# Performance work log

Hardware: AMD Instinct MI355X
Metric: run time of the kernel (lower is better)

The kernel has to match this reference:

```python
import jax, jax.numpy as jnp
import numpy as np

NUM_HEADS = 16
NUM_HIDDENS = 1024
NEG_INF = -1e6


def setup_inputs() -> dict:
    key = jax.random.key(0)
    ks = jax.random.split(key, 8)
    B, S, D = 2, 2048, NUM_HIDDENS
    scale = 1.0 / np.sqrt(D)
    return {
        "q": jax.random.normal(ks[0], (B, S, D), jnp.float32),
        "k": jax.random.normal(ks[1], (B, S, D), jnp.float32),
        "v": jax.random.normal(ks[2], (B, S, D), jnp.float32),
        # nn.Linear weights have shape (out_features, in_features)
        "Wq": jax.random.normal(ks[3], (D, D), jnp.float32) * scale,
        "Wk": jax.random.normal(ks[4], (D, D), jnp.float32) * scale,
        "Wv": jax.random.normal(ks[5], (D, D), jnp.float32) * scale,
        "Wo": jax.random.normal(ks[6], (D, D), jnp.float32) * scale,
        "valid_len": jax.random.randint(ks[7], (B,), 1, 2048 + 1, jnp.int32),
    }


def _unpack_heads(x, nh):
    # (B, S, H) -> (B*nh, S, H//nh), matching Unpack_base_head
    B, S, H = x.shape
    return x.reshape(B, S, nh, H // nh).transpose(0, 2, 1, 3).reshape(B * nh, S, H // nh)


def _merge_heads(x, nh):
    # Faithful to Merge_base_head: (B*nh, S, dh) -> (B, nh, S, dh)
    # -> permute(0,2,3,1) -> (B, S, dh, nh) -> (B, S, dh*nh)
    Bnh, S, dh = x.shape
    B = Bnh // nh
    x = x.reshape(B, nh, S, dh).transpose(0, 2, 3, 1)
    return x.reshape(B, S, dh * nh)


def reference(q, k, v, Wq, Wk, Wv, Wo, valid_len):
    nh = NUM_HEADS
    # projections (bias=False); Linear: x @ W.T
    qh = _unpack_heads(q @ Wq.T, nh)  # (B*nh, S, dh)
    kh = _unpack_heads(k @ Wk.T, nh)
    vh = _unpack_heads(v @ Wv.T, nh)
    dh = qh.shape[-1]
    scores = jnp.einsum("bqd,bkd->bqk", qh, kh) / jnp.sqrt(jnp.float32(dh))
    # repeat_interleave valid_len by num_heads along dim 0
    vl = jnp.repeat(valid_len, nh)  # (B*nh,)
    key_pos = jnp.arange(scores.shape[-1])  # (S,)
    mask = key_pos[None, None, :] < vl[:, None, None]  # (B*nh, 1, S)
    scores = jnp.where(mask, scores, NEG_INF)
    attn = jax.nn.softmax(scores, axis=-1)  # dropout=0.0 (eval) -> identity
    out = jnp.einsum("bqk,bkd->bqd", attn, vh)  # (B*nh, S, dh)
    out = _merge_heads(out, nh) @ Wo.T  # (B, S, H)
    return out, attn
```

## Files before the change

### kernel.cpp

```cpp
#include <hip/hip_runtime.h>
#include <stdint.h>

#define SB 2048
#define DB 1024
#define NHB 16
#define DHB 64

typedef __attribute__((ext_vector_type(8))) short short8;
typedef __attribute__((ext_vector_type(4))) short short4v;
typedef __attribute__((ext_vector_type(4))) float f32x4;

#define SC2 0.18033688011112042f

__device__ __forceinline__ unsigned short f2bf(float f) {
  union { float f; uint32_t u; } v; v.f = f;
  uint32_t u = v.u;
  return (unsigned short)((u + 0x7FFFu + ((u >> 16) & 1u)) >> 16);
}

__device__ __forceinline__ void gld16(const void* g, void* l) {
  __builtin_amdgcn_global_load_lds(
      (const __attribute__((address_space(1))) void*)g,
      (__attribute__((address_space(3))) void*)l, 16, 0, 0);
}

__device__ __forceinline__ int xcd_swz(int bid, int nwg) {
  return (bid & 7) * (nwg >> 3) + (bid >> 3);
}

struct ConvArgs {
  const float* s[7];
  unsigned short* d[7];
  int n[7];
};

__global__ __launch_bounds__(256) void conv_kernel(ConvArgs a) {
  const int t = blockIdx.y;
  const float* __restrict__ src = a.s[t];
  unsigned short* __restrict__ dst = a.d[t];
  const int n8 = a.n[t] >> 3;
  for (int i = blockIdx.x * 256 + threadIdx.x; i < n8; i += gridDim.x * 256) {
    const f32x4* p = (const f32x4*)src + (size_t)i * 2;
    f32x4 x = p[0], y = p[1];
    short8 o;
    o[0] = (short)f2bf(x[0]); o[1] = (short)f2bf(x[1]);
    o[2] = (short)f2bf(x[2]); o[3] = (short)f2bf(x[3]);
    o[4] = (short)f2bf(y[0]); o[5] = (short)f2bf(y[1]);
    o[6] = (short)f2bf(y[2]); o[7] = (short)f2bf(y[3]);
    *(short8*)(dst + (size_t)i * 8) = o;
  }
}

struct GemmArgs {
  const unsigned short* A[3];
  const unsigned short* B[3];
  void* O[3];
  int mode[3];
};

__global__ __launch_bounds__(256) void gemm128(GemmArgs ga) {
  __shared__ unsigned short SH[17408];
  unsigned short* Ab = SH;
  unsigned short* Bb = SH + 8192;

  const int z = blockIdx.y;
  const unsigned short* __restrict__ A = ga.A[z];
  const unsigned short* __restrict__ Bw = ga.B[z];
  const int mode = ga.mode[z];

  const int tid = threadIdx.x;
  const int w = tid >> 6, lane = tid & 63;
  const int g = lane >> 4, li = lane & 15;
  const int wm = w >> 1, wn = w & 1;
  const int l = xcd_swz(blockIdx.x, 256);
  const int m0 = (l >> 3) * 128, n0 = (l & 7) * 128;

  const int srow = lane >> 3;
  const int sg = (lane & 7) ^ srow;

  f32x4 acc[4][4];
  #pragma unroll
  for (int i = 0; i < 4; ++i)
    #pragma unroll
    for (int j = 0; j < 4; ++j)
      #pragma unroll
      for (int e = 0; e < 4; ++e) acc[i][j][e] = 0.f;

  for (int k0 = 0; k0 < DB; k0 += 64) {
    __syncthreads();
    #pragma unroll
    for (int i = 0; i < 4; ++i) {
      int c = w * 4 + i;
      gld16(A + (size_t)(m0 + c * 8 + srow) * DB + k0 + sg * 8, Ab + c * 512);
      gld16(Bw + (size_t)(n0 + c * 8 + srow) * DB + k0 + sg * 8, Bb + c * 512);
    }
    __syncthreads();
    short8 af[4][2], bf[4][2];
    #pragma unroll
    for (int mf = 0; mf < 4; ++mf)
      #pragma unroll
      for (int ks = 0; ks < 2; ++ks)
        af[mf][ks] = *(const short8*)&Ab[(wm * 64 + mf * 16 + li) * 64 +
                                         (((ks * 4 + g) ^ (li & 7)) << 3)];
    #pragma unroll
    for (int nf = 0; nf < 4; ++nf)
      #pragma unroll
      for (int ks = 0; ks < 2; ++ks)
        bf[nf][ks] = *(const short8*)&Bb[(wn * 64 + nf * 16 + li) * 64 +
                                         (((ks * 4 + g) ^ (li & 7)) << 3)];
    __builtin_amdgcn_s_setprio(1);
    #pragma unroll
    for (int ks = 0; ks < 2; ++ks)
      #pragma unroll
      for (int mf = 0; mf < 4; ++mf)
        #pragma unroll
        for (int nf = 0; nf < 4; ++nf)
          acc[mf][nf] = __builtin_amdgcn_mfma_f32_16x16x32_bf16(
              af[mf][ks], bf[nf][ks], acc[mf][nf], 0, 0, 0);
    __builtin_amdgcn_s_setprio(0);
  }

  if (mode == 0) {
    unsigned short* O = (unsigned short*)ga.O[z];
    #pragma unroll
    for (int mf = 0; mf < 4; ++mf)
      #pragma unroll
      for (int nf = 0; nf < 4; ++nf)
        #pragma unroll
        for (int r = 0; r < 4; ++r) {
          int row = m0 + wm * 64 + mf * 16 + g * 4 + r;
          int col = n0 + wn * 64 + nf * 16 + li;
          int b_ = row >> 11, s_ = row & 2047;
          int h = col >> 6, dp = col & 63;
          O[((size_t)(b_ * NHB + h) * SB + s_) * DHB + dp] = f2bf(acc[mf][nf][r]);
        }
  } else {
    unsigned short* O = (unsigned short*)ga.O[z];
    __syncthreads();
    #pragma unroll
    for (int mf = 0; mf < 4; ++mf)
      #pragma unroll
      for (int nf = 0; nf < 4; ++nf) {
        short4v pk;
        #pragma unroll
        for (int r = 0; r < 4; ++r) pk[r] = (short)f2bf(acc[mf][nf][r]);
        *(short4v*)&SH[(size_t)(wn * 64 + nf * 16 + li) * 136 +
                       wm * 64 + mf * 16 + g * 4] = pk;
      }
    __syncthreads();
    int c = tid >> 1, rh = tid & 1;
    int col = n0 + c;
    int h = col >> 6, dp = col & 63;
    int b_ = m0 >> 11, s0 = (m0 & 2047) + rh * 64;
    unsigned short* dst = O + ((size_t)(b_ * NHB + h) * DHB + dp) * SB + s0;
    #pragma unroll
    for (int j = 0; j < 8; ++j)
      *(short8*)(dst + j * 8) = *(const short8*)&SH[c * 136 + rh * 64 + j * 8];
  }
}

__global__ __launch_bounds__(256) void attn_kernel(
    const unsigned short* __restrict__ Qh, const unsigned short* __restrict__ Kh,
    const unsigned short* __restrict__ Vt, const int* __restrict__ valid_len,
    float* __restrict__ attn_out, unsigned short* __restrict__ Mg)
{
  __shared__ unsigned short Kb[4096];
  __shared__ unsigned short Vb[4096];
  __shared__ unsigned short QP[64][88];

  const int tid = threadIdx.x;
  const int wave = tid >> 6, lane = tid & 63;
  const int g = lane >> 4, li = lane & 15;
  const int lsw = xcd_swz(blockIdx.x, 1024);
  const int xcd = lsw >> 7, j = lsw & 127;
  const int bh = ((j >> 6) << 4) + xcd * 2 + ((j >> 5) & 1);
  const int q0 = (j & 31) * 64;
  const int b_ = bh >> 4;
  const int vl = valid_len[b_];
  const int nkt = min(32, (vl + 63) >> 6);

  const int srow = lane >> 3;
  const int sg = (lane & 7) ^ srow;

  {
    int qr = tid >> 2, cs = (tid & 3) * 16;
    const unsigned short* src = Qh + ((size_t)bh * SB + q0 + qr) * DHB + cs;
    *(short8*)&QP[qr][cs]     = *(const short8*)src;
    *(short8*)&QP[qr][cs + 8] = *(const short8*)(src + 8);
  }
  __syncthreads();

  short8 qa[2];
  #pragma unroll
  for (int ks = 0; ks < 2; ++ks)
    qa[ks] = *(const short8*)&QP[wave * 16 + li][ks * 32 + g * 8];

  float lQ = 0.f;

  for (int kti = 0; kti < nkt; ++kti) {
    const int kt = kti * 64;
    __syncthreads();
    {
      int c = wave * 2;
      gld16(Kh + ((size_t)bh * SB + kt + c * 8 + srow) * DHB + sg * 8,
            &Kb[c * 512]);
      gld16(Kh + ((size_t)bh * SB + kt + (c + 1) * 8 + srow) * DHB + sg * 8,
            &Kb[(c + 1) * 512]);
    }
    __syncthreads();
    f32x4 sc[4];
    #pragma unroll
    for (int nf = 0; nf < 4; ++nf)
      #pragma unroll
      for (int e = 0; e < 4; ++e) sc[nf][e] = 0.f;
    __builtin_amdgcn_s_setprio(1);
    #pragma unroll
    for (int ks = 0; ks < 2; ++ks)
      #pragma unroll
      for (int nf = 0; nf < 4; ++nf) {
        short8 kbf = *(const short8*)&Kb[(nf * 16 + li) * 64 +
                                         (((ks * 4 + g) ^ (li & 7)) << 3)];
        sc[nf] = __builtin_amdgcn_mfma_f32_16x16x32_bf16(kbf, qa[ks], sc[nf], 0, 0, 0);
      }
    __builtin_amdgcn_s_setprio(0);
    float la = 0.f;
    #pragma unroll
    for (int nf = 0; nf < 4; ++nf)
      #pragma unroll
      for (int r = 0; r < 4; ++r) {
        int key = kt + nf * 16 + g * 4 + r;
        float s2 = (key < vl) ? sc[nf][r] * SC2 : -1.5e6f;
        la += exp2f(s2);
      }
    lQ += la;
  }

  float L = lQ;
  L += __shfl_xor(L, 16);
  L += __shfl_xor(L, 32);
  const float rlQ = 1.f / L;

  f32x4 oacc[4];
  #pragma unroll
  for (int nf = 0; nf < 4; ++nf)
    #pragma unroll
    for (int e = 0; e < 4; ++e) oacc[nf][e] = 0.f;

  for (int kti = 0; kti < nkt; ++kti) {
    const int kt = kti * 64;
    __syncthreads();
    {
      int c = wave * 2;
      gld16(Kh + ((size_t)bh * SB + kt + c * 8 + srow) * DHB + sg * 8,
            &Kb[c * 512]);
      gld16(Kh + ((size_t)bh * SB + kt + (c + 1) * 8 + srow) * DHB + sg * 8,
            &Kb[(c + 1) * 512]);
      gld16(Vt + ((size_t)bh * DHB + c * 8 + srow) * SB + kt + sg * 8,
            &Vb[c * 512]);
      gld16(Vt + ((size_t)bh * DHB + (c + 1) * 8 + srow) * SB + kt + sg * 8,
            &Vb[(c + 1) * 512]);
    }
    __syncthreads();
    f32x4 sc[4];
    #pragma unroll
    for (int nf = 0; nf < 4; ++nf)
      #pragma unroll
      for (int e = 0; e < 4; ++e) sc[nf][e] = 0.f;
    __builtin_amdgcn_s_setprio(1);
    #pragma unroll
    for (int ks = 0; ks < 2; ++ks)
      #pragma unroll
      for (int nf = 0; nf < 4; ++nf) {
        short8 kbf = *(const short8*)&Kb[(nf * 16 + li) * 64 +
                                         (((ks * 4 + g) ^ (li & 7)) << 3)];
        sc[nf] = __builtin_amdgcn_mfma_f32_16x16x32_bf16(kbf, qa[ks], sc[nf], 0, 0, 0);
      }
    __builtin_amdgcn_s_setprio(0);
    {
      int qrow = q0 + wave * 16 + li;
      #pragma unroll
      for (int nf = 0; nf < 4; ++nf) {
        short4v pk;
        #pragma unroll
        for (int r = 0; r < 4; ++r) {
          int key = kt + nf * 16 + g * 4 + r;
          float s2 = (key < vl) ? sc[nf][r] * SC2 : -1.5e6f;
          float p = exp2f(s2) * rlQ;
          sc[nf][r] = p;
          pk[r] = (short)f2bf(p);
        }
        __builtin_nontemporal_store(
            sc[nf],
            (f32x4*)(attn_out + (size_t)bh * SB * SB + (size_t)qrow * SB +
                     kt + nf * 16 + g * 4));
        *(short4v*)&QP[wave * 16 + li][nf * 16 + g * 4] = pk;
      }
    }
    __builtin_amdgcn_s_setprio(1);
    #pragma unroll
    for (int ks = 0; ks < 2; ++ks) {
      short8 pa = *(const short8*)&QP[wave * 16 + li][ks * 32 + g * 8];
      #pragma unroll
      for (int nf = 0; nf < 4; ++nf) {
        short8 vbf = *(const short8*)&Vb[(nf * 16 + li) * 64 +
                                         (((ks * 4 + g) ^ (li & 7)) << 3)];
        oacc[nf] = __builtin_amdgcn_mfma_f32_16x16x32_bf16(pa, vbf, oacc[nf], 0, 0, 0);
      }
    }
    __builtin_amdgcn_s_setprio(0);
  }

  {
    int c0 = nkt * 64;
    int rem4 = (SB - c0) >> 2;
    if (rem4 > 0) {
      f32x4 z;
      z[0] = 0.f; z[1] = 0.f; z[2] = 0.f; z[3] = 0.f;
      for (int row = 0; row < 64; ++row) {
        float* dst = attn_out + (size_t)bh * SB * SB + (size_t)(q0 + row) * SB + c0;
        for (int c = tid; c < rem4; c += 256)
          __builtin_nontemporal_store(z, (f32x4*)dst + c);
      }
    }
  }

  const int h = bh & 15;
  #pragma unroll
  for (int nf = 0; nf < 4; ++nf)
    #pragma unroll
    for (int r = 0; r < 4; ++r) {
      int qrow = q0 + wave * 16 + g * 4 + r;
      int dp = nf * 16 + li;
      Mg[((size_t)b_ * SB + qrow) * DB + dp * NHB + h] = f2bf(oacc[nf][r]);
    }
}

__global__ __launch_bounds__(256) void outproj_kernel(
    const unsigned short* __restrict__ A, const unsigned short* __restrict__ Bw,
    float* __restrict__ Out)
{
  __shared__ unsigned short SH[12288];
  unsigned short* Ab = SH;
  unsigned short* Bb = SH + 8192;

  const int tid = threadIdx.x;
  const int w = tid >> 6, lane = tid & 63;
  const int g = lane >> 4, li = lane & 15;
  const int wm = w >> 1, wn = w & 1;
  const int l = xcd_swz(blockIdx.x, 512);
  const int m0 = (l >> 4) * 128, n0 = (l & 15) * 64;

  const int srow = lane >> 3;
  const int sg = (lane & 7) ^ srow;

  int a_off[4][2], b_off[2][2];
  #pragma unroll
  for (int mf = 0; mf < 4; ++mf) {
    int row = wm * 64 + mf * 16 + li;
    #pragma unroll
    for (int ks = 0; ks < 2; ++ks)
      a_off[mf][ks] = row * 64 + (((ks * 4 + g) ^ (li & 7)) << 3);
  }
  #pragma unroll
  for (int nf = 0; nf < 2; ++nf) {
    int row = wn * 32 + nf * 16 + li;
    #pragma unroll
    for (int ks = 0; ks < 2; ++ks)
      b_off[nf][ks] = row * 64 + (((ks * 4 + g) ^ (li & 7)) << 3);
  }

  f32x4 acc[4][2];
  #pragma unroll
  for (int i = 0; i < 4; ++i)
    #pragma unroll
    for (int j = 0; j < 2; ++j)
      #pragma unroll
      for (int e = 0; e < 4; ++e) acc[i][j][e] = 0.f;

  for (int k0 = 0; k0 < DB; k0 += 64) {
    __syncthreads();
    #pragma unroll
    for (int i = 0; i < 4; ++i) {
      int c = w * 4 + i;
      gld16(A + (size_t)(m0 + c * 8 + srow) * DB + k0 + sg * 8, Ab + c * 512);
    }
    #pragma unroll
    for (int i = 0; i < 2; ++i) {
      int c = w * 2 + i;
      gld16(Bw + (size_t)(n0 + c * 8 + srow) * DB + k0 + sg * 8, Bb + c * 512);
    }
    __syncthreads();
    short8 af[4][2], bf[2][2];
    #pragma unroll
    for (int mf = 0; mf < 4; ++mf)
      #pragma unroll
      for (int ks = 0; ks < 2; ++ks)
        af[mf][ks] = *(const short8*)&Ab[a_off[mf][ks]];
    #pragma unroll
    for (int nf = 0; nf < 2; ++nf)
      #pragma unroll
      for (int ks = 0; ks < 2; ++ks)
        bf[nf][ks] = *(const short8*)&Bb[b_off[nf][ks]];
    __builtin_amdgcn_s_setprio(1);
    #pragma unroll
    for (int ks = 0; ks < 2; ++ks)
      #pragma unroll
      for (int mf = 0; mf < 4; ++mf)
        #pragma unroll
        for (int nf = 0; nf < 2; ++nf)
          acc[mf][nf] = __builtin_amdgcn_mfma_f32_16x16x32_bf16(
              af[mf][ks], bf[nf][ks], acc[mf][nf], 0, 0, 0);
    __builtin_amdgcn_s_setprio(0);
  }

  #pragma unroll
  for (int mf = 0; mf < 4; ++mf)
    #pragma unroll
    for (int nf = 0; nf < 2; ++nf)
      #pragma unroll
      for (int r = 0; r < 4; ++r) {
        int row = m0 + wm * 64 + mf * 16 + g * 4 + r;
        int col = n0 + wn * 32 + nf * 16 + li;
        Out[(size_t)row * DB + col] = acc[mf][nf][r];
      }
}

extern "C" void kernel_launch(void* const* d_in, const int* in_sizes, int n_in,
                              void* d_out, int out_size, void* d_ws, size_t ws_size,
                              hipStream_t stream) {
  const float* q  = (const float*)d_in[0];
  const float* k  = (const float*)d_in[1];
  const float* v  = (const float*)d_in[2];
  const float* Wq = (const float*)d_in[3];
  const float* Wk = (const float*)d_in[4];
  const float* Wv = (const float*)d_in[5];
  const float* Wo = (const float*)d_in[6];
  const int* vlen = (const int*)d_in[7];

  const size_t HS = (size_t)2 * NHB * SB * DHB;
  const size_t WS = (size_t)DB * DB;

  unsigned short* ws = (unsigned short*)d_ws;
  unsigned short* qb  = ws;
  unsigned short* kb  = qb + HS;
  unsigned short* vb  = kb + HS;
  unsigned short* Wqb = vb + HS;
  unsigned short* Wkb = Wqb + WS;
  unsigned short* Wvb = Wkb + WS;
  unsigned short* Wob = Wvb + WS;
  unsigned short* Qh  = Wob + WS;
  unsigned short* Kh  = Qh + HS;
  unsigned short* Vt  = Kh + HS;
  unsigned short* Mg  = qb;

  float* out  = (float*)d_out;
  float* attn = out + (size_t)2 * SB * DB;

  ConvArgs ca;
  ca.s[0] = q;  ca.d[0] = qb;  ca.n[0] = (int)HS;
  ca.s[1] = k;  ca.d[1] = kb;  ca.n[1] = (int)HS;
  ca.s[2] = v;  ca.d[2] = vb;  ca.n[2] = (int)HS;
  ca.s[3] = Wq; ca.d[3] = Wqb; ca.n[3] = (int)WS;
  ca.s[4] = Wk; ca.d[4] = Wkb; ca.n[4] = (int)WS;
  ca.s[5] = Wv; ca.d[5] = Wvb; ca.n[5] = (int)WS;
  ca.s[6] = Wo; ca.d[6] = Wob; ca.n[6] = (int)WS;

  GemmArgs pa;
  pa.A[0] = qb;  pa.A[1] = kb;  pa.A[2] = vb;
  pa.B[0] = Wqb; pa.B[1] = Wkb; pa.B[2] = Wvb;
  pa.O[0] = Qh;  pa.O[1] = Kh;  pa.O[2] = Vt;
  pa.mode[0] = 0; pa.mode[1] = 0; pa.mode[2] = 1;

  dim3 blk(256);
  conv_kernel<<<dim3(1024, 7), blk, 0, stream>>>(ca);
  gemm128<<<dim3(256, 3), blk, 0, stream>>>(pa);
  attn_kernel<<<dim3(1024), blk, 0, stream>>>(Qh, Kh, Vt, vlen, attn, Mg);
  outproj_kernel<<<dim3(512), blk, 0, stream>>>(Mg, Wob, out);
}
```

Measured before the change: 235.7 us.

## Load K and V fragments directly from global memory, dropping LDS staging and barriers

The attention kernel no longer stages K and V tiles into shared memory with global_load_lds and block-wide barriers. Each wave now reads its MFMA operands straight from global memory (through the caches), and Q is loaded directly into registers. Only a small per-wave P buffer stays in LDS. This removes the __syncthreads pairs and the LDS footprint per iteration, but each of the four waves refetches the same K/V data from L1/L2 with less coalesced 16-byte loads, and the setprio hints are dropped.

New measurement: 280.0 us. +18.8%, slower.

```diff
diff --git a/kernel.cpp b/kernel.cpp
--- a/kernel.cpp
+++ b/kernel.cpp
@@ -164,9 +164,7 @@
     const unsigned short* __restrict__ Vt, const int* __restrict__ valid_len,
     float* __restrict__ attn_out, unsigned short* __restrict__ Mg)
 {
-  __shared__ unsigned short Kb[4096];
-  __shared__ unsigned short Vb[4096];
-  __shared__ unsigned short QP[64][88];
+  __shared__ unsigned short P[64][72];
 
   const int tid = threadIdx.x;
   const int wave = tid >> 6, lane = tid & 63;
@@ -179,50 +177,31 @@
   const int vl = valid_len[b_];
   const int nkt = min(32, (vl + 63) >> 6);
 
-  const int srow = lane >> 3;
-  const int sg = (lane & 7) ^ srow;
-
-  {
-    int qr = tid >> 2, cs = (tid & 3) * 16;
-    const unsigned short* src = Qh + ((size_t)bh * SB + q0 + qr) * DHB + cs;
-    *(short8*)&QP[qr][cs]     = *(const short8*)src;
-    *(short8*)&QP[qr][cs + 8] = *(const short8*)(src + 8);
-  }
-  __syncthreads();
-
+  const unsigned short* __restrict__ Kb = Kh + (size_t)bh * SB * DHB;
+  const unsigned short* __restrict__ Vb = Vt + (size_t)bh * DHB * SB;
+
+  const int qrow_l = q0 + wave * 16 + li;
   short8 qa[2];
-  #pragma unroll
-  for (int ks = 0; ks < 2; ++ks)
-    qa[ks] = *(const short8*)&QP[wave * 16 + li][ks * 32 + g * 8];
+  qa[0] = *(const short8*)(Qh + ((size_t)bh * SB + qrow_l) * DHB + g * 8);
+  qa[1] = *(const short8*)(Qh + ((size_t)bh * SB + qrow_l) * DHB + 32 + g * 8);
 
   float lQ = 0.f;
 
   for (int kti = 0; kti < nkt; ++kti) {
     const int kt = kti * 64;
-    __syncthreads();
-    {
-      int c = wave * 2;
-      gld16(Kh + ((size_t)bh * SB + kt + c * 8 + srow) * DHB + sg * 8,
-            &Kb[c * 512]);
-      gld16(Kh + ((size_t)bh * SB + kt + (c + 1) * 8 + srow) * DHB + sg * 8,
-            &Kb[(c + 1) * 512]);
-    }
-    __syncthreads();
     f32x4 sc[4];
     #pragma unroll
     for (int nf = 0; nf < 4; ++nf)
       #pragma unroll
       for (int e = 0; e < 4; ++e) sc[nf][e] = 0.f;
-    __builtin_amdgcn_s_setprio(1);
     #pragma unroll
     for (int ks = 0; ks < 2; ++ks)
       #pragma unroll
       for (int nf = 0; nf < 4; ++nf) {
-        short8 kbf = *(const short8*)&Kb[(nf * 16 + li) * 64 +
-                                         (((ks * 4 + g) ^ (li & 7)) << 3)];
+        short8 kbf = *(const short8*)(Kb + (size_t)(kt + nf * 16 + li) * DHB +
+                                      ks * 32 + g * 8);
         sc[nf] = __builtin_amdgcn_mfma_f32_16x16x32_bf16(kbf, qa[ks], sc[nf], 0, 0, 0);
       }
-    __builtin_amdgcn_s_setprio(0);
     float la = 0.f;
     #pragma unroll
     for (int nf = 0; nf < 4; ++nf)
@@ -248,36 +227,20 @@
 
   for (int kti = 0; kti < nkt; ++kti) {
     const int kt = kti * 64;
-    __syncthreads();
+    f32x4 sc[4];
+    #pragma unroll
+    for (int nf = 0; nf < 4; ++nf)
+      #pragma unroll
+      for (int e = 0; e < 4; ++e) sc[nf][e] = 0.f;
+    #pragma unroll
+    for (int ks = 0; ks < 2; ++ks)
+      #pragma unroll
+      for (int nf = 0; nf < 4; ++nf) {
+        short8 kbf = *(const short8*)(Kb + (size_t)(kt + nf * 16 + li) * DHB +
+                                      ks * 32 + g * 8);
+        sc[nf] = __builtin_amdgcn_mfma_f32_16x16x32_bf16(kbf, qa[ks], sc[nf], 0, 0, 0);
+      }
     {
-      int c = wave * 2;
-      gld16(Kh + ((size_t)bh * SB + kt + c * 8 + srow) * DHB + sg * 8,
-            &Kb[c * 512]);
-      gld16(Kh + ((size_t)bh * SB + kt + (c + 1) * 8 + srow) * DHB + sg * 8,
-            &Kb[(c + 1) * 512]);
-      gld16(Vt + ((size_t)bh * DHB + c * 8 + srow) * SB + kt + sg * 8,
-            &Vb[c * 512]);
-      gld16(Vt + ((size_t)bh * DHB + (c + 1) * 8 + srow) * SB + kt + sg * 8,
-            &Vb[(c + 1) * 512]);
-    }
-    __syncthreads();
-    f32x4 sc[4];
-    #pragma unroll
-    for (int nf = 0; nf < 4; ++nf)
-      #pragma unroll
-      for (int e = 0; e < 4; ++e) sc[nf][e] = 0.f;
-    __builtin_amdgcn_s_setprio(1);
-    #pragma unroll
-    for (int ks = 0; ks < 2; ++ks)
-      #pragma unroll
-      for (int nf = 0; nf < 4; ++nf) {
-        short8 kbf = *(const short8*)&Kb[(nf * 16 + li) * 64 +
-                                         (((ks * 4 + g) ^ (li & 7)) << 3)];
-        sc[nf] = __builtin_amdgcn_mfma_f32_16x16x32_bf16(kbf, qa[ks], sc[nf], 0, 0, 0);
-      }
-    __builtin_amdgcn_s_setprio(0);
-    {
-      int qrow = q0 + wave * 16 + li;
       #pragma unroll
       for (int nf = 0; nf < 4; ++nf) {
         short4v pk;
@@ -291,23 +254,21 @@
         }
         __builtin_nontemporal_store(
             sc[nf],
-            (f32x4*)(attn_out + (size_t)bh * SB * SB + (size_t)qrow * SB +
+            (f32x4*)(attn_out + (size_t)bh * SB * SB + (size_t)qrow_l * SB +
                      kt + nf * 16 + g * 4));
-        *(short4v*)&QP[wave * 16 + li][nf * 16 + g * 4] = pk;
-      }
-    }
-    __builtin_amdgcn_s_setprio(1);
+        *(short4v*)&P[wave * 16 + li][nf * 16 + g * 4] = pk;
+      }
+    }
     #pragma unroll
     for (int ks = 0; ks < 2; ++ks) {
-      short8 pa = *(const short8*)&QP[wave * 16 + li][ks * 32 + g * 8];
+      short8 pa = *(const short8*)&P[wave * 16 + li][ks * 32 + g * 8];
       #pragma unroll
       for (int nf = 0; nf < 4; ++nf) {
-        short8 vbf = *(const short8*)&Vb[(nf * 16 + li) * 64 +
-                                         (((ks * 4 + g) ^ (li & 7)) << 3)];
+        short8 vbf = *(const short8*)(Vb + (size_t)(nf * 16 + li) * SB + kt +
+                                      ks * 32 + g * 8);
         oacc[nf] = __builtin_amdgcn_mfma_f32_16x16x32_bf16(pa, vbf, oacc[nf], 0, 0, 0);
       }
     }
-    __builtin_amdgcn_s_setprio(0);
   }
 
   {
```
